# Kernel tuning notes

Hardware: AMD Instinct MI355X
Metric: run time of the kernel (lower is better)

Reference implementation:

```python
import jax, jax.numpy as jnp
import numpy as np

RACE_CYCLE = 1024
BET_AMOUNT = 131072
D1, D2 = 64, 16


def setup_inputs() -> dict:
    key = jax.random.key(0)
    ks = jax.random.split(key, 4)
    s1 = 1.0 / np.sqrt(RACE_CYCLE)
    s2 = 1.0 / np.sqrt(D1)
    s3 = 1.0 / np.sqrt(D2)
    return {
        "inputs": jax.random.normal(ks[0], (RACE_CYCLE, BET_AMOUNT), dtype=jnp.float32),
        "W1": jax.random.normal(ks[1], (RACE_CYCLE, D1), dtype=jnp.float32) * s1,
        "b1": jnp.zeros((D1,), dtype=jnp.float32),
        "W2": jax.random.normal(ks[2], (D1, D2), dtype=jnp.float32) * s2,
        "b2": jnp.zeros((D2,), dtype=jnp.float32),
        "W3": jax.random.normal(ks[3], (D2, 1), dtype=jnp.float32) * s3,
        "b3": jnp.zeros((1,), dtype=jnp.float32),
    }


def reference(inputs, W1, b1, W2, b2, W3, b3):
    # tf.map_fn over transposed rows == one batched MLP over inputs.T
    x = inputs.T                                # [bet_amount, race_cycle]
    h1 = jax.nn.relu(x @ W1 + b1)               # [bet_amount, 64]
    h2 = jax.nn.relu(h1 @ W2 + b2)              # [bet_amount, 16]
    out = (h2 @ W3 + b3)[:, 0]                  # [bet_amount]
    return out[None, :]                         # [1, bet_amount]
```

## Files before the change

### kernel.cpp

```cpp
#include <hip/hip_runtime.h>


#define RC 1024
#define BA 131072
#define D1 64
#define D2 16

#define MB  256
#define KC  32
#define NCH (RC / KC)
#define HS  33

using f16x8  = __attribute__((ext_vector_type(8))) _Float16;
using f32x16 = __attribute__((ext_vector_type(16))) float;

__global__ __launch_bounds__(512, 4) void mlp3_mfma_v3(
    const float* __restrict__ inputs,
    const float* __restrict__ W1,
    const float* __restrict__ b1,
    const float* __restrict__ W2,
    const float* __restrict__ b2,
    const float* __restrict__ W3,
    const float* __restrict__ b3,
    float* __restrict__ out)
{
    __shared__ __align__(16) float Ash[2][KC][MB];
    __shared__ __align__(16) f16x8 Wsh[2][4][64];

    const int t  = threadIdx.x;
    const int l  = t & 63;
    const int w  = t >> 6;
    const int ln = l & 31;
    const int hi = l >> 5;
    const int mBase = blockIdx.x * MB;

    const int wfrag = t >> 6;
    const int wks   = t >> 7;
    const int wnt   = (t >> 6) & 1;
    const int wlane = t & 63;
    const int wn    = (wlane & 31) + 32 * wnt;
    const int wkb   = wks * 16 + (wlane >> 5) * 8;

    float4 xr0, xr1, xr2, xr3;
    float  wr[8];

#define LOADA(c) { \
    const float* p_ = inputs + (size_t)((c) * KC + w * 4) * BA + (mBase + (l << 2)); \
    xr0 = *(const float4*)(p_); \
    xr1 = *(const float4*)(p_ + (size_t)BA); \
    xr2 = *(const float4*)(p_ + (size_t)2 * BA); \
    xr3 = *(const float4*)(p_ + (size_t)3 * BA); }

#define LOADW(c) { if (t < 256) { \
    const float* q_ = W1 + (size_t)((c) * KC + wkb) * D1 + wn; \
    _Pragma("unroll") for (int u = 0; u < 8; ++u) wr[u] = q_[(size_t)u * D1]; } }

#define WRITE(b) { \
    { float* d_ = &Ash[b][w * 4][l << 2]; \
      *(float4*)(d_)          = xr0; \
      *(float4*)(d_ + MB)     = xr1; \
      *(float4*)(d_ + 2 * MB) = xr2; \
      *(float4*)(d_ + 3 * MB) = xr3; } \
    if (t < 256) { \
      f16x8 h_; \
      _Pragma("unroll") for (int u = 0; u < 8; ++u) h_[u] = (_Float16)wr[u]; \
      Wsh[b][wfrag][wlane] = h_; } }

#define BAR() { asm volatile("s_waitcnt lgkmcnt(0)" ::: "memory"); \
                __builtin_amdgcn_s_barrier(); \
                __builtin_amdgcn_sched_barrier(0); }

    f32x16 acc0 = {};
    f32x16 acc1 = {};

#define COMPUTE(b) { \
    _Pragma("unroll") for (int ks = 0; ks < 2; ++ks) { \
      float av[8]; \
      _Pragma("unroll") for (int u = 0; u < 8; ++u) \
        av[u] = Ash[b][ks * 16 + hi * 8 + u][w * 32 + ln]; \
      f16x8 a_; \
      _Pragma("unroll") for (int u = 0; u < 8; ++u) a_[u] = (_Float16)av[u]; \
      f16x8 b0_ = Wsh[b][ks * 2 + 0][l]; \
      f16x8 b1_ = Wsh[b][ks * 2 + 1][l]; \
      acc0 = __builtin_amdgcn_mfma_f32_32x32x16_f16(a_, b0_, acc0, 0, 0, 0); \
      acc1 = __builtin_amdgcn_mfma_f32_32x32x16_f16(a_, b1_, acc1, 0, 0, 0); \
    } }

    LOADA(0); LOADW(0);
    WRITE(0);
    LOADA(1); LOADW(1);
    BAR();

    for (int c = 0; c < NCH; ++c) {
        const int cur = c & 1;
        if (c + 1 < NCH) { WRITE(cur ^ 1); }
        if (c + 2 < NCH) { LOADA(c + 2); LOADW(c + 2); }
        COMPUTE(cur);
        BAR();
    }
#undef LOADA
#undef LOADW
#undef WRITE
#undef COMPUTE

    float* Hw = (float*)Ash + w * (32 * HS);
    const int mc = ln;
    const int dh = hi;

    float h2[D2];
    #pragma unroll
    for (int e = 0; e < D2; ++e) h2[e] = (dh == 0) ? b2[e] : 0.f;

#define EPI(ACC, DBASE) { \
    _Pragma("unroll") for (int r = 0; r < 16; ++r) { \
        const int mr = (r & 3) + 8 * (r >> 2) + 4 * dh; \
        Hw[mr * HS + mc] = ACC[r]; \
    } \
    asm volatile("s_waitcnt lgkmcnt(0)" ::: "memory"); \
    __builtin_amdgcn_sched_barrier(0); \
    _Pragma("unroll") for (int dd = 0; dd < 16; ++dd) { \
        const int d = (DBASE) + dh * 16 + dd; \
        float h = Hw[mc * HS + dh * 16 + dd] + b1[d]; \
        h = h > 0.f ? h : 0.f; \
        _Pragma("unroll") for (int e = 0; e < D2; ++e) \
            h2[e] = fmaf(h, W2[d * D2 + e], h2[e]); \
    } \
    asm volatile("s_waitcnt lgkmcnt(0)" ::: "memory"); \
    __builtin_amdgcn_sched_barrier(0); }

    EPI(acc0, 0)
    EPI(acc1, 32)
#undef EPI
#undef BAR

    #pragma unroll
    for (int e = 0; e < D2; ++e) h2[e] += __shfl_xor(h2[e], 32, 64);

    float o = b3[0];
    #pragma unroll
    for (int e = 0; e < D2; ++e) {
        float h = h2[e] > 0.f ? h2[e] : 0.f;
        o = fmaf(h, W3[e], o);
    }
    if (l < 32)
        out[mBase + w * 32 + mc] = o;
}

extern "C" void kernel_launch(void* const* d_in, const int* in_sizes, int n_in,
                              void* d_out, int out_size, void* d_ws, size_t ws_size,
                              hipStream_t stream) {
    const float* inputs = (const float*)d_in[0];
    const float* W1     = (const float*)d_in[1];
    const float* b1     = (const float*)d_in[2];
    const float* W2     = (const float*)d_in[3];
    const float* b2     = (const float*)d_in[4];
    const float* W3     = (const float*)d_in[5];
    const float* b3     = (const float*)d_in[6];
    float* out = (float*)d_out;

    dim3 block(512);
    dim3 grid(BA / MB);
    mlp3_mfma_v3<<<grid, block, 0, stream>>>(inputs, W1, b1, W2, b2, W3, b3, out);
}
```

Before: 715.5 us.

## Load input tiles directly into LDS via global_load_lds with smaller blocks

Replaces the register-staged global-to-LDS copy of the input tiles with direct global_load_lds transfers. It also halves the block tile to 128 rows with 256 threads, which doubles the grid. The goal is to remove the register round-trip and the extra VGPR pressure, and to raise occupancy. In exchange the prefetch depth drops from two chunks in flight to one, and every iteration now waits on vmcnt(0) before the barrier, which may expose memory latency.

Measured after the change: 720.5 us. Within noise of the previous version (+0.7%).

```diff
diff --git a/kernel.cpp b/kernel.cpp
--- a/kernel.cpp
+++ b/kernel.cpp
@@ -1,4 +1,5 @@
 #include <hip/hip_runtime.h>
+#include <stdint.h>
 
 
 #define RC 1024
@@ -6,7 +7,7 @@
 #define D1 64
 #define D2 16
 
-#define MB  256
+#define MB  128
 #define KC  32
 #define NCH (RC / KC)
 #define HS  33
@@ -14,7 +15,14 @@
 using f16x8  = __attribute__((ext_vector_type(8))) _Float16;
 using f32x16 = __attribute__((ext_vector_type(16))) float;
 
-__global__ __launch_bounds__(512, 4) void mlp3_mfma_v3(
+__device__ __forceinline__ void gld16(const float* g, float* lds) {
+    __builtin_amdgcn_global_load_lds(
+        (const __attribute__((address_space(1))) void*)g,
+        (__attribute__((address_space(3))) void*)lds,
+        16, 0, 0);
+}
+
+__global__ __launch_bounds__(256, 4) void mlp3_mfma_v4(
     const float* __restrict__ inputs,
     const float* __restrict__ W1,
     const float* __restrict__ b1,
@@ -34,44 +42,34 @@
     const int hi = l >> 5;
     const int mBase = blockIdx.x * MB;
 
-    const int wfrag = t >> 6;
-    const int wks   = t >> 7;
-    const int wnt   = (t >> 6) & 1;
-    const int wlane = t & 63;
-    const int wn    = (wlane & 31) + 32 * wnt;
-    const int wkb   = wks * 16 + (wlane >> 5) * 8;
+    const int wks = w >> 1;
+    const int wnt = w & 1;
+    const int wn  = ln + 32 * wnt;
+    const int wkb = wks * 16 + hi * 8;
 
-    float4 xr0, xr1, xr2, xr3;
-    float  wr[8];
-
-#define LOADA(c) { \
-    const float* p_ = inputs + (size_t)((c) * KC + w * 4) * BA + (mBase + (l << 2)); \
-    xr0 = *(const float4*)(p_); \
-    xr1 = *(const float4*)(p_ + (size_t)BA); \
-    xr2 = *(const float4*)(p_ + (size_t)2 * BA); \
-    xr3 = *(const float4*)(p_ + (size_t)3 * BA); }
-
-#define LOADW(c) { if (t < 256) { \
-    const float* q_ = W1 + (size_t)((c) * KC + wkb) * D1 + wn; \
-    _Pragma("unroll") for (int u = 0; u < 8; ++u) wr[u] = q_[(size_t)u * D1]; } }
-
-#define WRITE(b) { \
-    { float* d_ = &Ash[b][w * 4][l << 2]; \
-      *(float4*)(d_)          = xr0; \
-      *(float4*)(d_ + MB)     = xr1; \
-      *(float4*)(d_ + 2 * MB) = xr2; \
-      *(float4*)(d_ + 3 * MB) = xr3; } \
-    if (t < 256) { \
-      f16x8 h_; \
-      _Pragma("unroll") for (int u = 0; u < 8; ++u) h_[u] = (_Float16)wr[u]; \
-      Wsh[b][wfrag][wlane] = h_; } }
-
-#define BAR() { asm volatile("s_waitcnt lgkmcnt(0)" ::: "memory"); \
-                __builtin_amdgcn_s_barrier(); \
-                __builtin_amdgcn_sched_barrier(0); }
-
+    float wr[8];
     f32x16 acc0 = {};
     f32x16 acc1 = {};
+
+#define LOADW(c) { \
+    const float* q_ = W1 + (size_t)((c) * KC + wkb) * D1 + wn; \
+    _Pragma("unroll") for (int u = 0; u < 8; ++u) wr[u] = q_[(size_t)u * D1]; }
+
+#define GLOADA(c, b) { \
+    const float* g_ = inputs + (size_t)((c) * KC + w * 8 + hi) * BA + (mBase + (ln << 2)); \
+    _Pragma("unroll") for (int r = 0; r < 4; ++r) \
+        gld16(g_ + (size_t)(2 * r) * BA, &Ash[b][w * 8 + 2 * r][0]); }
+
+#define WRITEW(b) { \
+    f16x8 h_; \
+    _Pragma("unroll") for (int u = 0; u < 8; ++u) h_[u] = (_Float16)wr[u]; \
+    Wsh[b][w][l] = h_; }
+
+#define SYNC() { \
+    asm volatile("s_waitcnt vmcnt(0) lgkmcnt(0)" ::: "memory"); \
+    __builtin_amdgcn_sched_barrier(0); \
+    __builtin_amdgcn_s_barrier(); \
+    __builtin_amdgcn_sched_barrier(0); }
 
 #define COMPUTE(b) { \
     _Pragma("unroll") for (int ks = 0; ks < 2; ++ks) { \
@@ -86,22 +84,23 @@
       acc1 = __builtin_amdgcn_mfma_f32_32x32x16_f16(a_, b1_, acc1, 0, 0, 0); \
     } }
 
-    LOADA(0); LOADW(0);
-    WRITE(0);
-    LOADA(1); LOADW(1);
-    BAR();
+    LOADW(0); GLOADA(0, 0);
+    WRITEW(0);
+    SYNC();
 
     for (int c = 0; c < NCH; ++c) {
         const int cur = c & 1;
-        if (c + 1 < NCH) { WRITE(cur ^ 1); }
-        if (c + 2 < NCH) { LOADA(c + 2); LOADW(c + 2); }
+        const int nxt = cur ^ 1;
+        if (c + 1 < NCH) { LOADW(c + 1); GLOADA(c + 1, nxt); }
         COMPUTE(cur);
-        BAR();
+        if (c + 1 < NCH) { WRITEW(nxt); }
+        SYNC();
     }
-#undef LOADA
 #undef LOADW
-#undef WRITE
+#undef GLOADA
+#undef WRITEW
 #undef COMPUTE
+#undef SYNC
 
     float* Hw = (float*)Ash + w * (32 * HS);
     const int mc = ln;
@@ -131,7 +130,6 @@
     EPI(acc0, 0)
     EPI(acc1, 32)
 #undef EPI
-#undef BAR
 
     #pragma unroll
     for (int e = 0; e < D2; ++e) h2[e] += __shfl_xor(h2[e], 32, 64);
@@ -158,7 +156,7 @@
     const float* b3     = (const float*)d_in[6];
     float* out = (float*)d_out;
 
-    dim3 block(512);
+    dim3 block(256);
     dim3 grid(BA / MB);
-    mlp3_mfma_v3<<<grid, block, 0, stream>>>(inputs, W1, b1, W2, b2, W3, b3, out);
+    mlp3_mfma_v4<<<grid, block, 0, stream>>>(inputs, W1, b1, W2, b2, W3, b3, out);
 }
```

## Store fp16 k-major tiles in LDS and halve block tile size

Applied to the files above, without the earlier changes.

Activations are now converted to fp16 before the LDS store and kept in a padded [m][k] layout, so each MFMA operand is one 16-byte vector LDS read instead of eight scalar reads plus conversions. W1 gets the same [n][k] fp16 layout. The block shrinks to 256 threads and 128 columns, and the loop is unrolled by two with ping-pong register buffers so the LDS buffer indices are fixed at compile time. The trade-off is that global loads become scalar (still coalesced across threads) rather than float4, and more smaller blocks are launched.

Result: no change. 715.3 us (-0.0%).

```diff
diff --git a/kernel.cpp b/kernel.cpp
--- a/kernel.cpp
+++ b/kernel.cpp
@@ -6,15 +6,16 @@
 #define D1 64
 #define D2 16
 
-#define MB  256
+#define MB  128
 #define KC  32
 #define NCH (RC / KC)
+#define KS  40
 #define HS  33
 
 using f16x8  = __attribute__((ext_vector_type(8))) _Float16;
 using f32x16 = __attribute__((ext_vector_type(16))) float;
 
-__global__ __launch_bounds__(512, 4) void mlp3_mfma_v3(
+__global__ __launch_bounds__(256, 4) void mlp3_mfma_v5(
     const float* __restrict__ inputs,
     const float* __restrict__ W1,
     const float* __restrict__ b1,
@@ -24,8 +25,8 @@
     const float* __restrict__ b3,
     float* __restrict__ out)
 {
-    __shared__ __align__(16) float Ash[2][KC][MB];
-    __shared__ __align__(16) f16x8 Wsh[2][4][64];
+    __shared__ __align__(16) _Float16 Ash[2][MB][KS];
+    __shared__ __align__(16) _Float16 Wsh[2][D1][KS];
 
     const int t  = threadIdx.x;
     const int l  = t & 63;
@@ -34,69 +35,64 @@
     const int hi = l >> 5;
     const int mBase = blockIdx.x * MB;
 
-    const int wfrag = t >> 6;
-    const int wks   = t >> 7;
-    const int wnt   = (t >> 6) & 1;
-    const int wlane = t & 63;
-    const int wn    = (wlane & 31) + 32 * wnt;
-    const int wkb   = wks * 16 + (wlane >> 5) * 8;
+    const int mA = t & (MB - 1);
+    const int kg = t >> 7;
+    const int nW  = t & 63;
+    const int kg2 = t >> 6;
 
-    float4 xr0, xr1, xr2, xr3;
-    float  wr[8];
+    float ra[16], wa[8], rb[16], wb[8];
+    f32x16 acc0 = {};
+    f32x16 acc1 = {};
 
-#define LOADA(c) { \
-    const float* p_ = inputs + (size_t)((c) * KC + w * 4) * BA + (mBase + (l << 2)); \
-    xr0 = *(const float4*)(p_); \
-    xr1 = *(const float4*)(p_ + (size_t)BA); \
-    xr2 = *(const float4*)(p_ + (size_t)2 * BA); \
-    xr3 = *(const float4*)(p_ + (size_t)3 * BA); }
+#define LOADA(c, R) { \
+    const float* p_ = inputs + (size_t)((c) * KC + kg * 8) * BA + (mBase + mA); \
+    _Pragma("unroll") for (int s = 0; s < 2; ++s) \
+      _Pragma("unroll") for (int u = 0; u < 8; ++u) \
+        R[s * 8 + u] = p_[(size_t)(s * 16 + u) * BA]; }
 
-#define LOADW(c) { if (t < 256) { \
-    const float* q_ = W1 + (size_t)((c) * KC + wkb) * D1 + wn; \
-    _Pragma("unroll") for (int u = 0; u < 8; ++u) wr[u] = q_[(size_t)u * D1]; } }
+#define LOADW(c, R) { \
+    const float* q_ = W1 + (size_t)((c) * KC + kg2 * 8) * D1 + nW; \
+    _Pragma("unroll") for (int u = 0; u < 8; ++u) R[u] = q_[(size_t)u * D1]; }
 
-#define WRITE(b) { \
-    { float* d_ = &Ash[b][w * 4][l << 2]; \
-      *(float4*)(d_)          = xr0; \
-      *(float4*)(d_ + MB)     = xr1; \
-      *(float4*)(d_ + 2 * MB) = xr2; \
-      *(float4*)(d_ + 3 * MB) = xr3; } \
-    if (t < 256) { \
+#define WRITE(b, RA, RW) { \
+    _Pragma("unroll") for (int s = 0; s < 2; ++s) { \
       f16x8 h_; \
-      _Pragma("unroll") for (int u = 0; u < 8; ++u) h_[u] = (_Float16)wr[u]; \
-      Wsh[b][wfrag][wlane] = h_; } }
+      _Pragma("unroll") for (int u = 0; u < 8; ++u) h_[u] = (_Float16)RA[s * 8 + u]; \
+      *(f16x8*)&Ash[b][mA][s * 16 + kg * 8] = h_; } \
+    { f16x8 h_; \
+      _Pragma("unroll") for (int u = 0; u < 8; ++u) h_[u] = (_Float16)RW[u]; \
+      *(f16x8*)&Wsh[b][nW][kg2 * 8] = h_; } }
 
 #define BAR() { asm volatile("s_waitcnt lgkmcnt(0)" ::: "memory"); \
+                __builtin_amdgcn_sched_barrier(0); \
                 __builtin_amdgcn_s_barrier(); \
                 __builtin_amdgcn_sched_barrier(0); }
 
-    f32x16 acc0 = {};
-    f32x16 acc1 = {};
-
 #define COMPUTE(b) { \
-    _Pragma("unroll") for (int ks = 0; ks < 2; ++ks) { \
-      float av[8]; \
-      _Pragma("unroll") for (int u = 0; u < 8; ++u) \
-        av[u] = Ash[b][ks * 16 + hi * 8 + u][w * 32 + ln]; \
-      f16x8 a_; \
-      _Pragma("unroll") for (int u = 0; u < 8; ++u) a_[u] = (_Float16)av[u]; \
-      f16x8 b0_ = Wsh[b][ks * 2 + 0][l]; \
-      f16x8 b1_ = Wsh[b][ks * 2 + 1][l]; \
+    _Pragma("unroll") for (int ks2 = 0; ks2 < 2; ++ks2) { \
+      f16x8 a_  = *(const f16x8*)&Ash[b][w * 32 + ln][ks2 * 16 + hi * 8]; \
+      f16x8 b0_ = *(const f16x8*)&Wsh[b][ln]         [ks2 * 16 + hi * 8]; \
+      f16x8 b1_ = *(const f16x8*)&Wsh[b][ln + 32]    [ks2 * 16 + hi * 8]; \
       acc0 = __builtin_amdgcn_mfma_f32_32x32x16_f16(a_, b0_, acc0, 0, 0, 0); \
       acc1 = __builtin_amdgcn_mfma_f32_32x32x16_f16(a_, b1_, acc1, 0, 0, 0); \
     } }
 
-    LOADA(0); LOADW(0);
-    WRITE(0);
-    LOADA(1); LOADW(1);
+    LOADA(0, ra); LOADW(0, wa);
+    WRITE(0, ra, wa);
+    LOADA(1, rb); LOADW(1, wb);
     BAR();
 
-    for (int c = 0; c < NCH; ++c) {
-        const int cur = c & 1;
-        if (c + 1 < NCH) { WRITE(cur ^ 1); }
-        if (c + 2 < NCH) { LOADA(c + 2); LOADW(c + 2); }
-        COMPUTE(cur);
+    for (int c = 0; c < NCH; c += 2) {
+        COMPUTE(0);
+        if (c + 1 < NCH) WRITE(1, rb, wb);
+        if (c + 2 < NCH) { LOADA(c + 2, ra); LOADW(c + 2, wa); }
         BAR();
+        if (c + 1 < NCH) {
+            COMPUTE(1);
+            if (c + 2 < NCH) WRITE(0, ra, wa);
+            if (c + 3 < NCH) { LOADA(c + 3, rb); LOADW(c + 3, wb); }
+            BAR();
+        }
     }
 #undef LOADA
 #undef LOADW
@@ -158,7 +154,7 @@
     const float* b3     = (const float*)d_in[6];
     float* out = (float*)d_out;
 
-    dim3 block(512);
+    dim3 block(256);
     dim3 grid(BA / MB);
-    mlp3_mfma_v3<<<grid, block, 0, stream>>>(inputs, W1, b1, W2, b2, W3, b3, out);
+    mlp3_mfma_v5<<<grid, block, 0, stream>>>(inputs, W1, b1, W2, b2, W3, b3, out);
 }
```
